# Optimization experiments

Measured on AMD Instinct MI355X. Metric: run time of the kernel, lower is better.

The kernel has to match this reference:

```python
import jax, jax.numpy as jnp
import numpy as np

B, T, H, W, CIN = 8, 10, 64, 64, 32
F = 64          # filters
KH, KW = 3, 3
G = 4           # num_gate_copies


def _conv(x, k):
    # x: (N,H,W,Cin), k: (kh,kw,Cin,Cout), SAME padding, stride 1
    return jax.lax.conv_general_dilated(
        x, k, window_strides=(1, 1), padding='SAME',
        dimension_numbers=('NHWC', 'HWIO', 'NHWC'))


def setup_inputs() -> dict:
    key = jax.random.key(0)
    k1, k2, k3, k4 = jax.random.split(key, 4)
    inputs = jax.random.normal(k1, (B, T, H, W, CIN), dtype=jnp.float32)
    label_values = jax.random.randint(k2, (B,), 0, G, dtype=jnp.int32)
    kernel = jax.random.normal(k3, (KH, KW, CIN, 4 * F), dtype=jnp.float32) * 0.05
    recurrent_kernel = jax.random.normal(k4, (G, KH, KW, F, 4 * F), dtype=jnp.float32) * 0.05
    # unit_forget_bias: zeros with forget-gate slice set to 1.0
    bias = jnp.zeros((G, 4 * F), dtype=jnp.float32).at[:, F:2 * F].set(1.0)
    return {"inputs": inputs, "label_values": label_values,
            "kernel": kernel, "recurrent_kernel": recurrent_kernel, "bias": bias}


def reference(inputs, label_values, kernel, recurrent_kernel, bias):
    b, t, h_dim, w_dim, _ = inputs.shape
    f = recurrent_kernel.shape[-1] // 4
    # Per-sample gather of expert recurrent kernel / bias (label-indexed)
    k_b = recurrent_kernel[label_values]   # (B, kh, kw, F, 4F)
    b_b = bias[label_values]               # (B, 4F)

    # vmapped per-sample batch=1 recurrent conv (faithful to map_fn semantics)
    per_sample_conv = jax.vmap(lambda hs, ks: _conv(hs[None], ks)[0])

    def step(carry, x_t):
        h, c = carry
        z = _conv(x_t, kernel) + per_sample_conv(h, k_b) + b_b[:, None, None, :]
        i = jax.nn.sigmoid(z[..., :f])
        fg = jax.nn.sigmoid(z[..., f:2 * f])
        g = jnp.tanh(z[..., 2 * f:3 * f])
        o = jax.nn.sigmoid(z[..., 3 * f:])
        c_new = fg * c + i * g
        h_new = o * jnp.tanh(c_new)
        return (h_new, c_new), h_new

    h0 = jnp.zeros((b, h_dim, w_dim, f), dtype=inputs.dtype)
    c0 = jnp.zeros_like(h0)
    xs = jnp.moveaxis(inputs, 1, 0)  # (T, B, H, W, Cin)
    _, ys = jax.lax.scan(step, (h0, c0), xs)
    return jnp.moveaxis(ys, 0, 1)    # (B, T, H, W, F)
```

## Files before the change

### kernel.cpp

```cpp
#include <hip/hip_runtime.h>


typedef __attribute__((ext_vector_type(8))) short short8v;
typedef __attribute__((ext_vector_type(4))) float f32x4;
typedef __attribute__((ext_vector_type(4))) unsigned int u32x4;
typedef unsigned short u16;

#define HS 808
#define HB 3200

__device__ __forceinline__ u16 f2bf(float x) {
    union { float f; unsigned u; } a; a.f = x;
    unsigned r = a.u + 0x7FFFu + ((a.u >> 16) & 1u);
    return (u16)(r >> 16);
}
__device__ __forceinline__ float sigf(float x) { return 1.0f / (1.0f + __expf(-x)); }
__device__ __forceinline__ float tanhf_(float x) {
    float e = __expf(2.0f * x);
    return 1.0f - 2.0f / (e + 1.0f);
}

__global__ __launch_bounds__(256)
void prep_w(const float* __restrict__ kern, const float* __restrict__ rk,
            u16* __restrict__ wt_in, u16* __restrict__ wt_rk,
            unsigned* __restrict__ flags) {
    int idx = blockIdx.x * 256 + threadIdx.x;
    if (idx < 1024) flags[idx] = 0u;
    if (idx >= 82944) return;
    const float* s;
    u16* dst;
    if (idx < 9216) {
        int co = idx & 255, ckb = idx >> 8;
        int tap = ckb >> 2, kb = ckb & 3;
        s = kern + (size_t)((tap << 5) + (kb << 3)) * 256 + co;
        dst = wt_in + (size_t)idx * 8;
    } else {
        int j = idx - 9216;
        int co = j & 255, rest = j >> 8;
        int kb = rest & 3, gc = rest >> 2;
        int g = gc / 18, cc = gc - g * 18;
        int tap = cc >> 1;
        int cib = (cc & 1) << 5;
        s = rk + (size_t)(((g * 9 + tap) << 6) + cib + (kb << 3)) * 256 + co;
        dst = wt_rk + (size_t)j * 8;
    }
    union { u16 u[8]; uint4 q; } o;
    #pragma unroll
    for (int i = 0; i < 8; ++i) o.u[i] = f2bf(s[i * 256]);
    *(uint4*)dst = o.q;
}

__device__ __forceinline__ void stageXf(const float* __restrict__ src,
                                        short* __restrict__ halX,
                                        int tid, int y0, int x0) {
    #pragma unroll 2
    for (int s = tid; s < 400; s += 256) {
        int pos = s >> 2, kb = s & 3;
        int hy = pos / 10, hx = pos - hy * 10;
        int gy = y0 + hy - 1, gx = x0 + hx - 1;
        union { u16 u[8]; short8v v; } o;
        o.v = (short8v){0,0,0,0,0,0,0,0};
        if ((unsigned)gy < 64u && (unsigned)gx < 64u) {
            const float* p = src + (((gy << 6) + gx) << 5) + (kb << 3);
            float4 a0 = *(const float4*)p;
            float4 a1 = *(const float4*)(p + 4);
            o.u[0] = f2bf(a0.x); o.u[1] = f2bf(a0.y);
            o.u[2] = f2bf(a0.z); o.u[3] = f2bf(a0.w);
            o.u[4] = f2bf(a1.x); o.u[5] = f2bf(a1.y);
            o.u[6] = f2bf(a1.z); o.u[7] = f2bf(a1.w);
        }
        *(short8v*)&halX[kb * 800 + pos * 8] = o.v;
    }
}

__global__ __launch_bounds__(256, 4)
void lstm_all(const float* __restrict__ xf,
              const u16* __restrict__ wt_in, const u16* __restrict__ wt_rk,
              const float* __restrict__ bias, const int* __restrict__ labels,
              u16* __restrict__ hb0, u16* __restrict__ hb1,
              float* __restrict__ out, unsigned* __restrict__ flags)
{
    __shared__ short hal[HB + 8 * HS];

    const int tid  = threadIdx.x;
    const int lane = tid & 63;
    const int w    = tid >> 6;
    const int pxh  = w >> 1;
    const int fq   = w & 1;
    const int bid  = blockIdx.x;
    const int fh   = bid & 1;
    const int tile = (bid >> 1) & 63;
    const int b    = bid >> 7;
    const int ty = tile >> 3, tx = tile & 7;
    const int y0 = ty << 3, x0 = tx << 3;
    const int g = labels[b];

    const int co_l = lane & 15;
    const int kbl  = lane >> 4;
    const int prow = (lane & 15) >> 3, pcol = lane & 7;
    const int f = (fh << 5) + (fq << 4) + co_l;

    float bv[4];
    #pragma unroll
    for (int n = 0; n < 4; ++n)
        bv[n] = bias[(g << 8) + (n << 6) + f];

    int aoffm[2];
    #pragma unroll
    for (int m = 0; m < 2; ++m)
        aoffm[m] = ((pxh << 2) + (m << 1) + prow) * 10 + pcol;

    int poff[2][4], loff[2][4];
    #pragma unroll
    for (int m = 0; m < 2; ++m)
        #pragma unroll
        for (int rr = 0; rr < 4; ++rr) {
            int pf = (kbl << 2) + rr;
            int ly = (pxh << 2) + (m << 1) + (pf >> 3);
            int lx = pf & 7;
            poff[m][rr] = ((((y0 + ly) << 6) + x0 + lx) << 6) + f;
            loff[m][rr] = HB + (f >> 3) * HS + ((ly + 1) * 10 + lx + 1) * 8 + (f & 7);
        }

    float cst[2][4];
    #pragma unroll
    for (int m = 0; m < 2; ++m)
        #pragma unroll
        for (int rr = 0; rr < 4; ++rr) cst[m][rr] = 0.0f;

    const float* xsrc = xf + ((size_t)b * 10 << 17);
    float*       ob0  = out + ((size_t)b * 10 << 18);
    unsigned*    myfl = flags + bid;

    for (int s = tid; s < 808; s += 256)
        *(short8v*)&hal[HB + s * 8] = (short8v){0,0,0,0,0,0,0,0};
    stageXf(xsrc, hal, tid, y0, x0);
    __syncthreads();

    for (int t = 0; t < 10; ++t) {
        u16* hw = ((t & 1) ? hb1 : hb0) + ((size_t)b << 18);

        f32x4 acc[2][4];
        #pragma unroll
        for (int n = 0; n < 4; ++n)
            #pragma unroll
            for (int m = 0; m < 2; ++m)
                acc[m][n] = (f32x4){bv[n], bv[n], bv[n], bv[n]};

        #pragma unroll 3
        for (int tap = 0; tap < 9; ++tap) {
            const int koff = (tap / 3) * 10 + (tap % 3);
            const u16* wb = wt_in + (size_t)((((tap << 2) + kbl) << 8) + f) * 8;
            short8v bfr[4], af[2];
            #pragma unroll
            for (int n = 0; n < 4; ++n)
                bfr[n] = *(const short8v*)&wb[(size_t)n << 9];
            #pragma unroll
            for (int m = 0; m < 2; ++m)
                af[m] = *(const short8v*)&hal[kbl * 800 + (aoffm[m] + koff) * 8];
            #pragma unroll
            for (int m = 0; m < 2; ++m)
                #pragma unroll
                for (int n = 0; n < 4; ++n)
                    acc[m][n] = __builtin_amdgcn_mfma_f32_16x16x32_bf16(af[m], bfr[n], acc[m][n], 0, 0, 0);
        }

        if (t > 0) {
            if (tid < 64) {
                bool valid = false; int fidx = 0;
                if (tid < 16) {
                    int k = tid >> 1;
                    int kk = k + (k >= 4);
                    int nty = ty + kk / 3 - 1, ntx = tx + kk % 3 - 1;
                    valid = (unsigned)nty < 8u && (unsigned)ntx < 8u;
                    fidx = (b << 7) + ((((nty << 3) + ntx) << 1) | (tid & 1));
                } else if (tid == 16) {
                    valid = true;
                    fidx = (b << 7) + (tile << 1) + (1 - fh);
                }
                unsigned tgt = (unsigned)t;
                int guard = 0;
                for (;;) {
                    unsigned vv = tgt;
                    if (valid)
                        vv = __hip_atomic_load(flags + fidx, __ATOMIC_RELAXED,
                                               __HIP_MEMORY_SCOPE_SYSTEM);
                    if (__all(vv >= tgt)) break;
                    if (++guard > (1 << 19)) break;
                    __builtin_amdgcn_s_sleep(2);
                }
            }
            __syncthreads();

            const u16* hr = ((t & 1) ? hb0 : hb1) + ((size_t)b << 18);
            #pragma unroll
            for (int u = 0; u < 2; ++u) {
                int s = tid + (u << 8);
                if (s < 288) {
                    int posr = s >> 3, kb = s & 7;
                    int hy, hx;
                    if (posr < 10)      { hy = 0; hx = posr; }
                    else if (posr < 20) { hy = 9; hx = posr - 10; }
                    else { int v = posr - 20; hy = 1 + (v >> 1); hx = (v & 1) * 9; }
                    int gy = y0 + hy - 1, gx = x0 + hx - 1;
                    bool inb = (unsigned)gy < 64u && (unsigned)gx < 64u;
                    const u16* ga = inb ? (hr + (((gy << 6) + gx) << 6) + (kb << 3)) : hr;
                    u32x4 v;
                    asm volatile("global_load_dwordx4 %0, %1, off sc0 sc1"
                                 : "=v"(v) : "v"(ga) : "memory");
                    asm volatile("s_waitcnt vmcnt(0)" ::: "memory");
                    __builtin_amdgcn_sched_barrier(0);
                    if (!inb) v = (u32x4){0u, 0u, 0u, 0u};
                    *(u32x4*)&hal[HB + kb * HS + (hy * 10 + hx) * 8] = v;
                }
            }
            {
                int px = tid >> 2;
                int kbu = ((1 - fh) << 2) + (tid & 3);
                int py = px >> 3, pxx = px & 7;
                const u16* ga = hr + ((((y0 + py) << 6) + x0 + pxx) << 6) + (kbu << 3);
                u32x4 v;
                asm volatile("global_load_dwordx4 %0, %1, off sc0 sc1"
                             : "=v"(v) : "v"(ga) : "memory");
                asm volatile("s_waitcnt vmcnt(0)" ::: "memory");
                __builtin_amdgcn_sched_barrier(0);
                *(u32x4*)&hal[HB + kbu * HS + ((py + 1) * 10 + pxx + 1) * 8] = v;
            }
            __syncthreads();

            #pragma unroll 3
            for (int c = 0; c < 18; ++c) {
                const int tap = c >> 1;
                const int koff = (tap / 3) * 10 + (tap % 3);
                const u16* wb = wt_rk + (size_t)(((((g * 18 + c) << 2) + kbl) << 8) + f) * 8;
                short8v bfr[4], af[2];
                #pragma unroll
                for (int n = 0; n < 4; ++n)
                    bfr[n] = *(const short8v*)&wb[(size_t)n << 9];
                const int abase = HB + (((c & 1) << 2) + kbl) * HS;
                #pragma unroll
                for (int m = 0; m < 2; ++m)
                    af[m] = *(const short8v*)&hal[abase + (aoffm[m] + koff) * 8];
                #pragma unroll
                for (int m = 0; m < 2; ++m)
                    #pragma unroll
                    for (int n = 0; n < 4; ++n)
                        acc[m][n] = __builtin_amdgcn_mfma_f32_16x16x32_bf16(af[m], bfr[n], acc[m][n], 0, 0, 0);
            }
        }
        __syncthreads();

        float* ob = ob0 + ((size_t)t << 18);
        #pragma unroll
        for (int m = 0; m < 2; ++m) {
            #pragma unroll
            for (int rr = 0; rr < 4; ++rr) {
                float zi = acc[m][0][rr], zf = acc[m][1][rr];
                float zg = acc[m][2][rr], zo = acc[m][3][rr];
                float cn = sigf(zf) * cst[m][rr] + sigf(zi) * tanhf_(zg);
                float hn = sigf(zo) * tanhf_(cn);
                cst[m][rr] = cn;
                ob[poff[m][rr]] = hn;
                hal[loff[m][rr]] = (short)f2bf(hn);
            }
        }
        __syncthreads();

        if (t < 9) {
            {
                int px = tid >> 2;
                int kbu = (fh << 2) + (tid & 3);
                int py = px >> 3, pxx = px & 7;
                u32x4 v = *(const u32x4*)&hal[HB + kbu * HS + ((py + 1) * 10 + pxx + 1) * 8];
                const u16* ga = hw + ((((y0 + py) << 6) + x0 + pxx) << 6) + (kbu << 3);
                asm volatile("global_store_dwordx4 %0, %1, off sc0 sc1"
                             :: "v"(ga), "v"(v) : "memory");
            }
            stageXf(xsrc + ((size_t)(t + 1) << 17), hal, tid, y0, x0);
            asm volatile("s_waitcnt vmcnt(0)" ::: "memory");
            __syncthreads();
            if (tid == 0)
                __hip_atomic_fetch_add(myfl, 1u, __ATOMIC_RELAXED,
                                       __HIP_MEMORY_SCOPE_SYSTEM);
        }
    }
}

extern "C" void kernel_launch(void* const* d_in, const int* in_sizes, int n_in,
                              void* d_out, int out_size, void* d_ws, size_t ws_size,
                              hipStream_t stream)
{
    const float* x    = (const float*)d_in[0];
    const int*   lbl  = (const int*)  d_in[1];
    const float* kern = (const float*)d_in[2];
    const float* rk   = (const float*)d_in[3];
    const float* bias = (const float*)d_in[4];
    float* out = (float*)d_out;

    u16* hb0   = (u16*)d_ws;
    u16* hb1   = hb0 + 2097152;
    u16* wt_in = hb1 + 2097152;
    u16* wt_rk = wt_in + 73728;
    unsigned* flags = (unsigned*)(wt_rk + 589824);

    hipLaunchKernelGGL(prep_w, dim3(324), dim3(256), 0, stream,
                       kern, rk, wt_in, wt_rk, flags);

    hipLaunchKernelGGL(lstm_all, dim3(1024), dim3(256), 0, stream,
                       x, wt_in, wt_rk, bias, lbl, hb0, hb1, out, flags);
}
```

Measured before the change: 202.3 us.

## Give each block all filters of a 4x8 tile to halve halo exchange

Each block previously owned an 8x8 spatial tile and half of the 64 filters. It now owns a 4x8 tile with all filters, so 16x8 tiles per sample replace 8x8 tiles times two filter halves. This removes the cross-block exchange of the other filter half, shrinks LDS use, and means only the tile border of h is written to and read from global memory each step. The neighbor flag wait now covers 8 spatial neighbors with no partner block. The cost is a larger halo relative to the interior (6x10 around 4x8) and more redundant x staging per output pixel.

```diff
diff --git a/kernel.cpp b/kernel.cpp
--- a/kernel.cpp
+++ b/kernel.cpp
@@ -6,8 +6,8 @@
 typedef __attribute__((ext_vector_type(4))) unsigned int u32x4;
 typedef unsigned short u16;
 
-#define HS 808
-#define HB 3200
+#define KS 488
+#define HB 1952
 
 __device__ __forceinline__ u16 f2bf(float x) {
     union { float f; unsigned u; } a; a.f = x;
@@ -53,9 +53,8 @@
 __device__ __forceinline__ void stageXf(const float* __restrict__ src,
                                         short* __restrict__ halX,
                                         int tid, int y0, int x0) {
-    #pragma unroll 2
-    for (int s = tid; s < 400; s += 256) {
-        int pos = s >> 2, kb = s & 3;
+    if (tid < 240) {
+        int pos = tid >> 2, kb = tid & 3;
         int hy = pos / 10, hx = pos - hy * 10;
         int gy = y0 + hy - 1, gx = x0 + hx - 1;
         union { u16 u[8]; short8v v; } o;
@@ -69,7 +68,7 @@
             o.u[4] = f2bf(a1.x); o.u[5] = f2bf(a1.y);
             o.u[6] = f2bf(a1.z); o.u[7] = f2bf(a1.w);
         }
-        *(short8v*)&halX[kb * 800 + pos * 8] = o.v;
+        *(short8v*)&halX[kb * KS + pos * 8] = o.v;
     }
 }
 
@@ -80,25 +79,22 @@
               u16* __restrict__ hb0, u16* __restrict__ hb1,
               float* __restrict__ out, unsigned* __restrict__ flags)
 {
-    __shared__ short hal[HB + 8 * HS];
+    __shared__ short hal[HB + 8 * KS];
 
     const int tid  = threadIdx.x;
     const int lane = tid & 63;
-    const int w    = tid >> 6;
-    const int pxh  = w >> 1;
-    const int fq   = w & 1;
+    const int wq   = tid >> 6;
     const int bid  = blockIdx.x;
-    const int fh   = bid & 1;
-    const int tile = (bid >> 1) & 63;
     const int b    = bid >> 7;
+    const int tile = bid & 127;
     const int ty = tile >> 3, tx = tile & 7;
-    const int y0 = ty << 3, x0 = tx << 3;
+    const int y0 = ty << 2, x0 = tx << 3;
     const int g = labels[b];
 
     const int co_l = lane & 15;
     const int kbl  = lane >> 4;
     const int prow = (lane & 15) >> 3, pcol = lane & 7;
-    const int f = (fh << 5) + (fq << 4) + co_l;
+    const int f = (wq << 4) + co_l;
 
     float bv[4];
     #pragma unroll
@@ -108,7 +104,7 @@
     int aoffm[2];
     #pragma unroll
     for (int m = 0; m < 2; ++m)
-        aoffm[m] = ((pxh << 2) + (m << 1) + prow) * 10 + pcol;
+        aoffm[m] = ((m << 1) + prow) * 10 + pcol;
 
     int poff[2][4], loff[2][4];
     #pragma unroll
@@ -116,11 +112,27 @@
         #pragma unroll
         for (int rr = 0; rr < 4; ++rr) {
             int pf = (kbl << 2) + rr;
-            int ly = (pxh << 2) + (m << 1) + (pf >> 3);
+            int ly = (m << 1) + (pf >> 3);
             int lx = pf & 7;
             poff[m][rr] = ((((y0 + ly) << 6) + x0 + lx) << 6) + f;
-            loff[m][rr] = HB + (f >> 3) * HS + ((ly + 1) * 10 + lx + 1) * 8 + (f & 7);
-        }
+            loff[m][rr] = HB + (f >> 3) * KS + ((ly + 1) * 10 + lx + 1) * 8 + (f & 7);
+        }
+
+    const bool okI = tid < 224;
+    int ilA = 0;
+    bool inA = false;
+    long offA = 0;
+    if (okI) {
+        int posr = tid >> 3, kb = tid & 7;
+        int hy, hx;
+        if (posr < 10)      { hy = 0; hx = posr; }
+        else if (posr < 20) { hy = 5; hx = posr - 10; }
+        else { int v = posr - 20; hy = 1 + (v >> 1); hx = (v & 1) * 9; }
+        int gy = y0 + hy - 1, gx = x0 + hx - 1;
+        inA = (unsigned)gy < 64u && (unsigned)gx < 64u;
+        offA = inA ? (long)((((gy << 6) + gx) << 6) + (kb << 3)) : 0;
+        ilA = HB + kb * KS + (hy * 10 + hx) * 8;
+    }
 
     float cst[2][4];
     #pragma unroll
@@ -132,7 +144,7 @@
     float*       ob0  = out + ((size_t)b * 10 << 18);
     unsigned*    myfl = flags + bid;
 
-    for (int s = tid; s < 808; s += 256)
+    for (int s = tid; s < 488; s += 256)
         *(short8v*)&hal[HB + s * 8] = (short8v){0,0,0,0,0,0,0,0};
     stageXf(xsrc, hal, tid, y0, x0);
     __syncthreads();
@@ -157,7 +169,7 @@
                 bfr[n] = *(const short8v*)&wb[(size_t)n << 9];
             #pragma unroll
             for (int m = 0; m < 2; ++m)
-                af[m] = *(const short8v*)&hal[kbl * 800 + (aoffm[m] + koff) * 8];
+                af[m] = *(const short8v*)&hal[kbl * KS + (aoffm[m] + koff) * 8];
             #pragma unroll
             for (int m = 0; m < 2; ++m)
                 #pragma unroll
@@ -168,15 +180,11 @@
         if (t > 0) {
             if (tid < 64) {
                 bool valid = false; int fidx = 0;
-                if (tid < 16) {
-                    int k = tid >> 1;
-                    int kk = k + (k >= 4);
+                if (tid < 8) {
+                    int kk = tid + (tid >= 4);
                     int nty = ty + kk / 3 - 1, ntx = tx + kk % 3 - 1;
-                    valid = (unsigned)nty < 8u && (unsigned)ntx < 8u;
-                    fidx = (b << 7) + ((((nty << 3) + ntx) << 1) | (tid & 1));
-                } else if (tid == 16) {
-                    valid = true;
-                    fidx = (b << 7) + (tile << 1) + (1 - fh);
+                    valid = (unsigned)nty < 16u && (unsigned)ntx < 8u;
+                    fidx = (b << 7) + (nty << 3) + ntx;
                 }
                 unsigned tgt = (unsigned)t;
                 int guard = 0;
@@ -192,39 +200,16 @@
             }
             __syncthreads();
 
-            const u16* hr = ((t & 1) ? hb0 : hb1) + ((size_t)b << 18);
-            #pragma unroll
-            for (int u = 0; u < 2; ++u) {
-                int s = tid + (u << 8);
-                if (s < 288) {
-                    int posr = s >> 3, kb = s & 7;
-                    int hy, hx;
-                    if (posr < 10)      { hy = 0; hx = posr; }
-                    else if (posr < 20) { hy = 9; hx = posr - 10; }
-                    else { int v = posr - 20; hy = 1 + (v >> 1); hx = (v & 1) * 9; }
-                    int gy = y0 + hy - 1, gx = x0 + hx - 1;
-                    bool inb = (unsigned)gy < 64u && (unsigned)gx < 64u;
-                    const u16* ga = inb ? (hr + (((gy << 6) + gx) << 6) + (kb << 3)) : hr;
-                    u32x4 v;
-                    asm volatile("global_load_dwordx4 %0, %1, off sc0 sc1"
-                                 : "=v"(v) : "v"(ga) : "memory");
-                    asm volatile("s_waitcnt vmcnt(0)" ::: "memory");
-                    __builtin_amdgcn_sched_barrier(0);
-                    if (!inb) v = (u32x4){0u, 0u, 0u, 0u};
-                    *(u32x4*)&hal[HB + kb * HS + (hy * 10 + hx) * 8] = v;
-                }
-            }
-            {
-                int px = tid >> 2;
-                int kbu = ((1 - fh) << 2) + (tid & 3);
-                int py = px >> 3, pxx = px & 7;
-                const u16* ga = hr + ((((y0 + py) << 6) + x0 + pxx) << 6) + (kbu << 3);
-                u32x4 v;
+            if (okI) {
+                const u16* hr = ((t & 1) ? hb0 : hb1) + ((size_t)b << 18);
+                u32x4 vA;
+                const u16* gaA = hr + offA;
                 asm volatile("global_load_dwordx4 %0, %1, off sc0 sc1"
-                             : "=v"(v) : "v"(ga) : "memory");
+                             : "=v"(vA) : "v"(gaA) : "memory");
                 asm volatile("s_waitcnt vmcnt(0)" ::: "memory");
                 __builtin_amdgcn_sched_barrier(0);
-                *(u32x4*)&hal[HB + kbu * HS + ((py + 1) * 10 + pxx + 1) * 8] = v;
+                if (!inA) vA = (u32x4){0u, 0u, 0u, 0u};
+                *(u32x4*)&hal[ilA] = vA;
             }
             __syncthreads();
 
@@ -237,7 +222,7 @@
                 #pragma unroll
                 for (int n = 0; n < 4; ++n)
                     bfr[n] = *(const short8v*)&wb[(size_t)n << 9];
-                const int abase = HB + (((c & 1) << 2) + kbl) * HS;
+                const int abase = HB + (((c & 1) << 2) + kbl) * KS;
                 #pragma unroll
                 for (int m = 0; m < 2; ++m)
                     af[m] = *(const short8v*)&hal[abase + (aoffm[m] + koff) * 8];
@@ -267,12 +252,14 @@
         __syncthreads();
 
         if (t < 9) {
-            {
-                int px = tid >> 2;
-                int kbu = (fh << 2) + (tid & 3);
-                int py = px >> 3, pxx = px & 7;
-                u32x4 v = *(const u32x4*)&hal[HB + kbu * HS + ((py + 1) * 10 + pxx + 1) * 8];
-                const u16* ga = hw + ((((y0 + py) << 6) + x0 + pxx) << 6) + (kbu << 3);
+            if (tid < 160) {
+                int pxr = tid >> 3, kb = tid & 7;
+                int dy, dx;
+                if (pxr < 8)       { dy = 0; dx = pxr; }
+                else if (pxr < 16) { dy = 3; dx = pxr - 8; }
+                else { int v = pxr - 16; dy = 1 + (v >> 1); dx = (v & 1) * 7; }
+                u32x4 v = *(const u32x4*)&hal[HB + kb * KS + ((dy + 1) * 10 + dx + 1) * 8];
+                const u16* ga = hw + ((((y0 + dy) << 6) + x0 + dx) << 6) + (kb << 3);
                 asm volatile("global_store_dwordx4 %0, %1, off sc0 sc1"
                              :: "v"(ga), "v"(v) : "memory");
             }
```

Result: faster. 188.2 us (-7.0%).
